# Performance work log

Measured on AMD Instinct MI355X. Metric: run time of the kernel, lower is better.

## Reference

```python
import jax, jax.numpy as jnp
import numpy as np

B, FEAT, SPD_H, CTRL_H, N_CMD = 32768, 512, 128, 256, 4


def _p(key, shape, fan_in):
    # torch nn.Linear default init: U(-1/sqrt(fan_in), 1/sqrt(fan_in))
    lim = 1.0 / np.sqrt(fan_in)
    return jax.random.uniform(key, shape, jnp.float32, -lim, lim)


def setup_inputs() -> dict:
    key = jax.random.key(0)
    ks = iter(jax.random.split(key, 32))
    inp = {
        "feat": jax.random.normal(next(ks), (B, FEAT), jnp.float32),
        "speed": jax.random.uniform(next(ks), (B,), jnp.float32),
        "command": jax.random.randint(next(ks), (B,), 0, N_CMD, jnp.int32),
        "ms_w1": _p(next(ks), (1, SPD_H), 1), "ms_b1": _p(next(ks), (SPD_H,), 1),
        "ms_w2": _p(next(ks), (SPD_H, SPD_H), SPD_H), "ms_b2": _p(next(ks), (SPD_H,), SPD_H),
        "ms_w3": _p(next(ks), (SPD_H, SPD_H), SPD_H), "ms_b3": _p(next(ks), (SPD_H,), SPD_H),
        # speed_pred_module: 512 -> 256 -> 256 -> 1
        "sp_w1": _p(next(ks), (FEAT, CTRL_H), FEAT), "sp_b1": _p(next(ks), (CTRL_H,), FEAT),
        "sp_w2": _p(next(ks), (CTRL_H, CTRL_H), CTRL_H), "sp_b2": _p(next(ks), (CTRL_H,), CTRL_H),
        "sp_w3": _p(next(ks), (CTRL_H, 1), CTRL_H), "sp_b3": _p(next(ks), (1,), CTRL_H),
        # join_module: Linear(640, 512)
        "join_w": _p(next(ks), (FEAT + SPD_H, FEAT), FEAT + SPD_H),
        "join_b": _p(next(ks), (FEAT,), FEAT + SPD_H),
        # 4 control heads: 512 -> 256 -> 256 -> 3 (stacked on expert axis e)
        "ctrl_w1": _p(next(ks), (N_CMD, FEAT, CTRL_H), FEAT), "ctrl_b1": _p(next(ks), (N_CMD, CTRL_H), FEAT),
        "ctrl_w2": _p(next(ks), (N_CMD, CTRL_H, CTRL_H), CTRL_H), "ctrl_b2": _p(next(ks), (N_CMD, CTRL_H), CTRL_H),
        "ctrl_w3": _p(next(ks), (N_CMD, CTRL_H, 3), CTRL_H), "ctrl_b3": _p(next(ks), (N_CMD, 3), CTRL_H),
    }
    return inp


def _mlp(x, w1, b1, w2, b2, w3, b3):
    # FullyConnectedNet: Linear, ReLU, Linear, Dropout(p=0 -> noop), ReLU, Linear
    h = jax.nn.relu(x @ w1 + b1)
    h = jax.nn.relu(h @ w2 + b2)
    return h @ w3 + b3


def reference(feat, speed, command,
              ms_w1, ms_b1, ms_w2, ms_b2, ms_w3, ms_b3,
              sp_w1, sp_b1, sp_w2, sp_b2, sp_w3, sp_b3,
              join_w, join_b,
              ctrl_w1, ctrl_b1, ctrl_w2, ctrl_b2, ctrl_w3, ctrl_b3):
    v = _mlp(speed[:, None], ms_w1, ms_b1, ms_w2, ms_b2, ms_w3, ms_b3)      # [B,128]
    joined = jnp.concatenate([feat, v], axis=1) @ join_w + join_b           # [B,512]
    v_p = _mlp(feat, sp_w1, sp_b1, sp_w2, sp_b2, sp_w3, sp_b3)              # [B,1]
    # command-indexed dispatch: compute all 4 heads densely, then select per sample
    h1 = jax.nn.relu(jnp.einsum('bd,edh->beh', joined, ctrl_w1) + ctrl_b1)  # [B,4,256]
    h2 = jax.nn.relu(jnp.einsum('beh,ehk->bek', h1, ctrl_w2) + ctrl_b2)     # [B,4,256]
    act_all = jnp.einsum('bek,eko->beo', h2, ctrl_w3) + ctrl_b3             # [B,4,3]
    action = jnp.take_along_axis(act_all, command[:, None, None].astype(jnp.int32), axis=1)[:, 0]  # [B,3]
    throttle = jax.nn.sigmoid(action[:, 0])
    steering = jnp.tanh(action[:, 1])
    brake = jax.nn.sigmoid(action[:, 2])
    return v_p, throttle, brake, steering
```

## Files before the change

kernel.cpp:

```cpp
#include <hip/hip_runtime.h>
#include <hip/hip_bf16.h>
#include <stdint.h>
#include <math.h>

#define BB 32768
#define FEAT 512
#define SPD_H 128
#define CTRL_H 256
#define NCMD 4

typedef __attribute__((ext_vector_type(8))) short bf16x8;
typedef __attribute__((ext_vector_type(4))) float f32x4;

__device__ __forceinline__ unsigned short f2bf(float f) {
  union { float f; uint32_t u; } v; v.f = f;
  uint32_t u = v.u;
  return (unsigned short)((u + 0x7fffu + ((u >> 16) & 1u)) >> 16);
}

__device__ __forceinline__ void async16(const unsigned short* g, unsigned short* l) {
  __builtin_amdgcn_global_load_lds(
      (const __attribute__((address_space(1))) unsigned int*)g,
      (__attribute__((address_space(3))) unsigned int*)l, 16, 0, 0);
}

__device__ __forceinline__ void gemm128(
    const unsigned short* __restrict__ A, int lda,
    const int* __restrict__ perm, int m_start, int m_cnt,
    const unsigned short* __restrict__ W, const float* __restrict__ bi,
    unsigned short* __restrict__ C, int ldc, int relu, int K, int mt, int nt) {
  extern __shared__ __align__(16) unsigned char dynsm[];
  unsigned short* As = (unsigned short*)dynsm;
  unsigned short* Bs = As + 128 * 32;

  const int m0 = mt * 128;
  if (m0 >= m_cnt) return;
  const int n0 = nt * 128;
  const int t = threadIdx.x;
  const int w = t >> 6, lane = t & 63;
  const int wm = w & 1, wn = w >> 1;

  f32x4 acc[4][4];
#pragma unroll
  for (int i = 0; i < 4; ++i)
#pragma unroll
    for (int j = 0; j < 4; ++j)
#pragma unroll
      for (int r = 0; r < 4; ++r) acc[i][j][r] = 0.f;

  const int fr = lane & 15;
  const int fk = (lane >> 4) * 8;

  const unsigned short* agp[2]; const unsigned short* bgp[2];
  unsigned short* al[2]; unsigned short* bl[2];
#pragma unroll
  for (int it = 0; it < 2; ++it) {
    int row = w * 32 + it * 16 + (lane >> 2);
    int seg8 = (lane & 3) * 8;
    int rl = m0 + row;
    if (rl >= m_cnt) rl = m_cnt - 1;
    int grow = perm ? perm[m_start + rl] : (m_start + rl);
    agp[it] = A + (size_t)grow * lda + seg8;
    bgp[it] = W + (size_t)(n0 + row) * K + seg8;
    al[it] = As + (w * 32 + it * 16) * 32;
    bl[it] = Bs + (w * 32 + it * 16) * 32;
  }

  for (int k0 = 0; k0 < K; k0 += 32) {
#pragma unroll
    for (int it = 0; it < 2; ++it) {
      async16(agp[it] + k0, al[it]);
      async16(bgp[it] + k0, bl[it]);
    }
    __syncthreads();
    bf16x8 af[4], bfv[4];
#pragma unroll
    for (int i = 0; i < 4; ++i)
      af[i] = *(const bf16x8*)(As + (wm * 64 + i * 16 + fr) * 32 + fk);
#pragma unroll
    for (int j = 0; j < 4; ++j)
      bfv[j] = *(const bf16x8*)(Bs + (wn * 64 + j * 16 + fr) * 32 + fk);
#pragma unroll
    for (int i = 0; i < 4; ++i)
#pragma unroll
      for (int j = 0; j < 4; ++j)
        acc[i][j] = __builtin_amdgcn_mfma_f32_16x16x32_bf16(af[i], bfv[j], acc[i][j], 0, 0, 0);
    __syncthreads();
  }

  const int rquad = (lane >> 4) * 4;
  const int cidx = lane & 15;

  float bv[4];
#pragma unroll
  for (int j = 0; j < 4; ++j) bv[j] = bi ? bi[n0 + wn * 64 + j * 16 + cidx] : 0.f;

  unsigned short (*bscr)[136] = (unsigned short(*)[136])dynsm;
#pragma unroll
  for (int c = 0; c < 4; ++c) {
    if (wm == (c >> 1)) {
#pragma unroll
      for (int j = 0; j < 4; ++j) {
#pragma unroll
        for (int ii = 0; ii < 2; ++ii) {
          int i = 2 * (c & 1) + ii;
          int lr = ii * 16 + rquad;
#pragma unroll
          for (int r = 0; r < 4; ++r) {
            float v = acc[i][j][r] + bv[j];
            if (relu) v = fmaxf(v, 0.f);
            bscr[lr + r][wn * 64 + j * 16 + cidx] = f2bf(v);
          }
        }
      }
    }
    __syncthreads();
#pragma unroll
    for (int q = 0; q < 2; ++q) {
      int sg = t + 256 * q;
      int lr = sg >> 4, cs = (sg & 15) * 8;
      int grow = m0 + c * 32 + lr;
      if (grow < m_cnt)
        *(bf16x8*)(C + (size_t)(m_start + grow) * ldc + (n0 + cs)) =
            *(const bf16x8*)(&bscr[lr][cs]);
    }
    __syncthreads();
  }
}

struct WSeg { const float* src; unsigned short* dst; int K; int N; int ldd; };
struct PrepArgs {
  WSeg s[12];
  int start[13];
  const float* join_w; unsigned short* wjbf;
  const float* feat; unsigned short* ajoin;
  const int* cmd; int* wavecnt;
  const float* join_b; const float* ctrl_w1; const float* ctrl_b1; float* b_f;
};
__launch_bounds__(256)
__global__ void k_prep(PrepArgs a) {
  int bx = blockIdx.x, t = threadIdx.x;
  if (bx < 16384) {
    int idx = bx * 256 + t;
    int i = idx >> 7;
    int j4 = (idx & 127) << 2;
    float4 f = *(const float4*)(a.feat + (size_t)i * FEAT + j4);
    ushort4 o;
    o.x = f2bf(f.x); o.y = f2bf(f.y); o.z = f2bf(f.z); o.w = f2bf(f.w);
    *(ushort4*)(a.ajoin + (size_t)i * 640 + j4) = o;
    return;
  }
  int rel = bx - 16384;
  if (rel < 320) {
    int idx = rel * 256 + t;
    float4 f = *(const float4*)(a.join_w + (size_t)idx * 4);
    ushort4 o;
    o.x = f2bf(f.x); o.y = f2bf(f.y); o.z = f2bf(f.z); o.w = f2bf(f.w);
    *(ushort4*)(a.wjbf + (size_t)idx * 4) = o;
    return;
  }
  rel -= 320;
  if (rel < a.start[12]) {
    __shared__ float tb[32][33];
    int si = 0;
    while (rel >= a.start[si + 1]) ++si;
    WSeg sg = a.s[si];
    int tile = rel - a.start[si];
    int tkx = sg.K >> 5;
    int tn = tile / tkx;
    int tk = tile - tn * tkx;
    int k0 = tk * 32, n0 = tn * 32;
    int tx = t & 31, ty = t >> 5;
#pragma unroll
    for (int j = 0; j < 4; ++j)
      tb[ty + j * 8][tx] = sg.src[(size_t)(k0 + ty + j * 8) * sg.N + n0 + tx];
    __syncthreads();
#pragma unroll
    for (int j = 0; j < 4; ++j)
      sg.dst[(size_t)(n0 + ty + j * 8) * sg.ldd + k0 + tx] = f2bf(tb[tx][ty + j * 8]);
    return;
  }
  rel -= a.start[12];
  if (rel < 128) {
    int i = rel * 256 + t;
    int c = a.cmd[i];
    int wid = i >> 6;
    int lane = t & 63;
#pragma unroll
    for (int cv = 0; cv < NCMD; ++cv) {
      unsigned long long m = __ballot(c == cv);
      if (lane == 0) a.wavecnt[cv * 512 + wid] = __popcll(m);
    }
    return;
  }
  int e = rel - 128;
  float s = a.ctrl_b1[e * 256 + t];
  const float* w = a.ctrl_w1 + (size_t)e * 512 * 256 + t;
  for (int m = 0; m < 512; ++m) s = fmaf(a.join_b[m], w[(size_t)m * 256], s);
  a.b_f[e * 256 + t] = s;
}

struct MidArgs {
  const int* cmd; const int* wavecnt; int* perm; int* offs;
  const unsigned short* c_w1t; const unsigned short* wjbf; unsigned short* wf_t;
  const float* speed;
  const float* ms_w1; const float* ms_b1;
  const unsigned short* ms_w2t; const float* ms_b2;
  const unsigned short* ms_w3t; const float* ms_b3;
  unsigned short* ajoin;
};
__launch_bounds__(256)
__global__ void k_mid(MidArgs a) {
  int b = blockIdx.x, t = threadIdx.x;
  if (b >= 168) {
    extern __shared__ __align__(16) unsigned char dynsm[];
    unsigned short (*hw)[136] = (unsigned short(*)[136])dynsm;
    unsigned short* BsM = (unsigned short*)(dynsm + 128 * 136 * 2);
    const int m0 = (b - 168) * 128;
    const int w = t >> 6, lane = t & 63;
    const int wm = w & 1, wn = w >> 1;
    const int fr = lane & 15, fk = (lane >> 4) * 8;
    const int rquad = (lane >> 4) * 4, cidx = lane & 15;
    {
      int r = t >> 1, half = t & 1;
      float s = a.speed[m0 + r];
#pragma unroll
      for (int c0 = 0; c0 < 64; c0 += 4) {
        int c = half * 64 + c0;
        float4 wv = *(const float4*)(a.ms_w1 + c);
        float4 bv = *(const float4*)(a.ms_b1 + c);
        hw[r][c + 0] = f2bf(fmaxf(fmaf(s, wv.x, bv.x), 0.f));
        hw[r][c + 1] = f2bf(fmaxf(fmaf(s, wv.y, bv.y), 0.f));
        hw[r][c + 2] = f2bf(fmaxf(fmaf(s, wv.z, bv.z), 0.f));
        hw[r][c + 3] = f2bf(fmaxf(fmaf(s, wv.w, bv.w), 0.f));
      }
    }
    __syncthreads();
    for (int layer = 0; layer < 2; ++layer) {
      const unsigned short* Wt = layer ? a.ms_w3t : a.ms_w2t;
      const float* bb = layer ? a.ms_b3 : a.ms_b2;
      f32x4 acc[4][4];
#pragma unroll
      for (int i = 0; i < 4; ++i)
#pragma unroll
        for (int j = 0; j < 4; ++j)
#pragma unroll
          for (int r = 0; r < 4; ++r) acc[i][j][r] = 0.f;
      for (int k0 = 0; k0 < 128; k0 += 32) {
#pragma unroll
        for (int it = 0; it < 2; ++it) {
          int row = w * 32 + it * 16 + (lane >> 2);
          async16(Wt + (size_t)row * 128 + k0 + (lane & 3) * 8,
                  BsM + (w * 32 + it * 16) * 32);
        }
        __syncthreads();
        bf16x8 af[4], bfv[4];
#pragma unroll
        for (int i = 0; i < 4; ++i)
          af[i] = *(const bf16x8*)(&hw[wm * 64 + i * 16 + fr][k0 + fk]);
#pragma unroll
        for (int j = 0; j < 4; ++j)
          bfv[j] = *(const bf16x8*)(BsM + (wn * 64 + j * 16 + fr) * 32 + fk);
#pragma unroll
        for (int i = 0; i < 4; ++i)
#pragma unroll
          for (int j = 0; j < 4; ++j)
            acc[i][j] = __builtin_amdgcn_mfma_f32_16x16x32_bf16(af[i], bfv[j], acc[i][j], 0, 0, 0);
        __syncthreads();
      }
#pragma unroll
      for (int j = 0; j < 4; ++j) {
        int col = wn * 64 + j * 16 + cidx;
        float bv = bb[col];
#pragma unroll
        for (int i = 0; i < 4; ++i) {
          int row = wm * 64 + i * 16 + rquad;
#pragma unroll
          for (int r = 0; r < 4; ++r) {
            float v = acc[i][j][r] + bv;
            if (layer == 0) v = fmaxf(v, 0.f);
            hw[row + r][col] = f2bf(v);
          }
        }
      }
      __syncthreads();
    }
    {
      int r = t >> 1, half = t & 1;
#pragma unroll
      for (int c8 = 0; c8 < 8; ++c8)
        *(bf16x8*)(a.ajoin + (size_t)(m0 + r) * 640 + 512 + half * 64 + c8 * 8) =
            *(const bf16x8*)(&hw[r][half * 64 + c8 * 8]);
    }
    return;
  }
  if (b >= 128) {
    int idx = b - 128;
    int mt = idx & 7, nt = idx >> 3;
    gemm128(a.c_w1t, 512, nullptr, 0, 1024, a.wjbf, nullptr, a.wf_t, 640, 0, 512, mt, nt);
    return;
  }
  __shared__ int pf[NCMD][4];
  __shared__ int tot[NCMD];
  int c = t >> 6, lane = t & 63;
  int v[8]; int s = 0;
#pragma unroll
  for (int q = 0; q < 8; ++q) { v[q] = a.wavecnt[c * 512 + lane * 8 + q]; s += v[q]; }
  int p = s;
#pragma unroll
  for (int m = 1; m < 64; m <<= 1) { int o = __shfl_up(p, m, 64); if (lane >= m) p += o; }
  int excl = p - s;
  if (lane == 63) tot[c] = p;
  if (lane == ((4 * b) >> 3)) {
    int base_off = (4 * b) & 7;
    int run = excl;
#pragma unroll
    for (int q = 0; q < 8; ++q) {
      if (q >= base_off && q < base_off + 4) pf[c][q - base_off] = run;
      run += v[q];
    }
  }
  __syncthreads();
  int soffs[NCMD + 1];
  soffs[0] = 0;
#pragma unroll
  for (int e = 0; e < NCMD; ++e) soffs[e + 1] = soffs[e] + tot[e];
  if (b == 0 && t == 0)
    for (int e = 0; e <= NCMD; ++e) a.offs[e] = soffs[e];
  int i = b * 256 + t;
  int mc = a.cmd[i];
  int lwid = t >> 6;
  int rank = 0, base = 0;
#pragma unroll
  for (int cv = 0; cv < NCMD; ++cv) {
    unsigned long long m = __ballot(mc == cv);
    if (mc == cv) {
      rank = __popcll(m & ((1ull << lane) - 1ull));
      base = soffs[cv] + pf[cv][lwid];
    }
  }
  a.perm[base + rank] = i;
}

struct MainArgs {
  const unsigned short* ajoin;
  const unsigned short* wf_t; const float* b_f;
  const unsigned short* sp_w1t; const float* sp_b1;
  unsigned short* ch1; unsigned short* sph1p;
  const int* perm; const int* seg;
};
__launch_bounds__(256)
__global__ void k_main(MainArgs a) {
  const int e = blockIdx.z;
  const int gid = blockIdx.x;
  const int mt = gid & 255, nt = gid >> 8;
  int ms = a.seg[e], mc = a.seg[e + 1] - ms;
  if (nt < 2) {
    gemm128(a.ajoin, 640, a.perm, ms, mc, a.wf_t + (size_t)e * 256 * 640,
            a.b_f + e * 256, a.ch1, 256, 1, 640, mt, nt);
  } else {
    gemm128(a.ajoin, 640, a.perm, ms, mc, a.sp_w1t, a.sp_b1,
            a.sph1p, 256, 1, 512, mt, nt - 2);
  }
}

struct VArgs {
  const unsigned short* A_s; const unsigned short* A_c;
  const unsigned short* W_s; const unsigned short* W_c;
  const float* b_s; const float* b_c;
  const float* w3_s; const float* b3_s;
  const float* w3_c; const float* b3_c;
  const int* perm; const int* seg;
  float* out;
};
__launch_bounds__(256)
__global__ void k_vgemm(VArgs a) {
  __shared__ unsigned short As[64 * 32];
  __shared__ unsigned short Bs[256 * 32];
  const int z = blockIdx.z;
  const unsigned short* A; const unsigned short* W; const float* bi;
  int m_start, m_cnt;
  if (z == 4) { A = a.A_s; W = a.W_s; bi = a.b_s; m_start = 0; m_cnt = BB; }
  else {
    A = a.A_c; W = a.W_c + (size_t)z * 65536; bi = a.b_c + z * 256;
    m_start = a.seg[z]; m_cnt = a.seg[z + 1] - m_start;
  }
  const int m0 = blockIdx.x * 64;
  if (m0 >= m_cnt) return;
  const int t = threadIdx.x, w = t >> 6, lane = t & 63;
  const int fr = lane & 15, fk = (lane >> 4) * 8;

  f32x4 acc[16];
#pragma unroll
  for (int j = 0; j < 16; ++j)
#pragma unroll
    for (int r = 0; r < 4; ++r) acc[j][r] = 0.f;

  int arow = m0 + w * 16 + (lane >> 2);
  if (arow >= m_cnt) arow = m_cnt - 1;
  const unsigned short* ap = A + (size_t)(m_start + arow) * 256 + (lane & 3) * 8;
  unsigned short* al = As + (w * 16) * 32;
  const unsigned short* bp[4]; unsigned short* bl[4];
#pragma unroll
  for (int it = 0; it < 4; ++it) {
    int brow = w * 64 + it * 16 + (lane >> 2);
    bp[it] = W + (size_t)brow * 256 + (lane & 3) * 8;
    bl[it] = Bs + (w * 64 + it * 16) * 32;
  }

  for (int k0 = 0; k0 < 256; k0 += 32) {
    async16(ap + k0, al);
#pragma unroll
    for (int it = 0; it < 4; ++it) async16(bp[it] + k0, bl[it]);
    __syncthreads();
    bf16x8 af = *(const bf16x8*)(As + (w * 16 + fr) * 32 + fk);
#pragma unroll
    for (int j = 0; j < 16; ++j) {
      bf16x8 bfv = *(const bf16x8*)(Bs + (j * 16 + fr) * 32 + fk);
      acc[j] = __builtin_amdgcn_mfma_f32_16x16x32_bf16(af, bfv, acc[j], 0, 0, 0);
    }
    __syncthreads();
  }

  const int rquad = (lane >> 4) * 4;
  float bcol[16];
#pragma unroll
  for (int j = 0; j < 16; ++j) bcol[j] = bi[j * 16 + fr];

  if (z == 4) {
    float aw[16];
#pragma unroll
    for (int j = 0; j < 16; ++j) aw[j] = a.w3_s[j * 16 + fr];
#pragma unroll
    for (int r = 0; r < 4; ++r) {
      float s = 0.f;
#pragma unroll
      for (int j = 0; j < 16; ++j)
        s = fmaf(fmaxf(acc[j][r] + bcol[j], 0.f), aw[j], s);
      s += __shfl_xor(s, 1, 64);
      s += __shfl_xor(s, 2, 64);
      s += __shfl_xor(s, 4, 64);
      s += __shfl_xor(s, 8, 64);
      int row = m0 + w * 16 + rquad + r;
      if (fr == 0 && row < m_cnt)
        a.out[a.perm[row]] = s + a.b3_s[0];
    }
  } else {
    float aw0[16], aw1[16], aw2[16];
#pragma unroll
    for (int j = 0; j < 16; ++j) {
      const float* wp = a.w3_c + (size_t)z * 768 + (j * 16 + fr) * 3;
      aw0[j] = wp[0]; aw1[j] = wp[1]; aw2[j] = wp[2];
    }
#pragma unroll
    for (int r = 0; r < 4; ++r) {
      float s0 = 0.f, s1 = 0.f, s2 = 0.f;
#pragma unroll
      for (int j = 0; j < 16; ++j) {
        float v = fmaxf(acc[j][r] + bcol[j], 0.f);
        s0 = fmaf(v, aw0[j], s0);
        s1 = fmaf(v, aw1[j], s1);
        s2 = fmaf(v, aw2[j], s2);
      }
#pragma unroll
      for (int m = 1; m <= 8; m <<= 1) {
        s0 += __shfl_xor(s0, m, 64);
        s1 += __shfl_xor(s1, m, 64);
        s2 += __shfl_xor(s2, m, 64);
      }
      int row = m0 + w * 16 + rquad + r;
      if (fr == 0 && row < m_cnt) {
        int orig = a.perm[m_start + row];
        float a0 = s0 + a.b3_c[z * 3 + 0];
        float a1 = s1 + a.b3_c[z * 3 + 1];
        float a2 = s2 + a.b3_c[z * 3 + 2];
        a.out[BB + orig]     = 1.f / (1.f + __expf(-a0));
        a.out[2 * BB + orig] = 1.f / (1.f + __expf(-a2));
        a.out[3 * BB + orig] = tanhf(a1);
      }
    }
  }
}

static inline size_t align256(size_t x) { return (x + 255) & ~(size_t)255; }

extern "C" void kernel_launch(void* const* d_in, const int* in_sizes, int n_in,
                              void* d_out, int out_size, void* d_ws, size_t ws_size,
                              hipStream_t stream) {
  const float* feat   = (const float*)d_in[0];
  const float* speed  = (const float*)d_in[1];
  const int*   command= (const int*)d_in[2];
  const float* ms_w1  = (const float*)d_in[3];
  const float* ms_b1  = (const float*)d_in[4];
  const float* ms_w2  = (const float*)d_in[5];
  const float* ms_b2  = (const float*)d_in[6];
  const float* ms_w3  = (const float*)d_in[7];
  const float* ms_b3  = (const float*)d_in[8];
  const float* sp_w1  = (const float*)d_in[9];
  const float* sp_b1  = (const float*)d_in[10];
  const float* sp_w2  = (const float*)d_in[11];
  const float* sp_b2  = (const float*)d_in[12];
  const float* sp_w3  = (const float*)d_in[13];
  const float* sp_b3  = (const float*)d_in[14];
  const float* join_w = (const float*)d_in[15];
  const float* join_b = (const float*)d_in[16];
  const float* ctrl_w1= (const float*)d_in[17];
  const float* ctrl_b1= (const float*)d_in[18];
  const float* ctrl_w2= (const float*)d_in[19];
  const float* ctrl_b2= (const float*)d_in[20];
  const float* ctrl_w3= (const float*)d_in[21];
  const float* ctrl_b3= (const float*)d_in[22];
  float* out = (float*)d_out;

  char* ws = (char*)d_ws;
  size_t off = 0;
  auto alloc = [&](size_t bytes) -> char* { char* p = ws + off; off = align256(off + bytes); return p; };

  unsigned short* ajoin  = (unsigned short*)alloc((size_t)BB * 640 * 2);
  unsigned short* sph1p  = (unsigned short*)alloc((size_t)BB * 256 * 2);
  unsigned short* ch1    = (unsigned short*)alloc((size_t)BB * 256 * 2);
  unsigned short* wtp    = (unsigned short*)alloc(1998848ull * 2);
  int* perm    = (int*)alloc((size_t)BB * 4);
  int* cnt     = (int*)alloc(64);
  int* wavecnt = (int*)alloc(4 * 512 * 4);
  float* b_f   = (float*)alloc(4 * 256 * 4);

  unsigned short* sp_w1t = wtp;
  unsigned short* sp_w2t = wtp + 131072;
  unsigned short* ms_w2t = wtp + 196608;
  unsigned short* ms_w3t = wtp + 212992;
  unsigned short* c_w1t  = wtp + 229376;
  unsigned short* c_w2t  = wtp + 753664;
  unsigned short* wjbf   = wtp + 1015808;
  unsigned short* wf_t   = wtp + 1343488;

  PrepArgs P;
  P.s[0] = { sp_w1, sp_w1t, 512, 256, 512 };
  P.s[1] = { sp_w2, sp_w2t, 256, 256, 256 };
  P.s[2] = { ms_w2, ms_w2t, 128, 128, 128 };
  P.s[3] = { ms_w3, ms_w3t, 128, 128, 128 };
  for (int e = 0; e < 4; ++e) P.s[4 + e] = { ctrl_w1 + (size_t)e * 512 * 256, c_w1t + (size_t)e * 131072, 512, 256, 512 };
  for (int e = 0; e < 4; ++e) P.s[8 + e] = { ctrl_w2 + (size_t)e * 256 * 256, c_w2t + (size_t)e * 65536, 256, 256, 256 };
  P.start[0] = 0;
  for (int i = 0; i < 12; ++i)
    P.start[i + 1] = P.start[i] + (P.s[i].K >> 5) * (P.s[i].N >> 5);
  P.join_w = join_w; P.wjbf = wjbf;
  P.feat = feat; P.ajoin = ajoin;
  P.cmd = command; P.wavecnt = wavecnt;
  P.join_b = join_b; P.ctrl_w1 = ctrl_w1; P.ctrl_b1 = ctrl_b1; P.b_f = b_f;
  int prep_blocks = 16384 + 320 + P.start[12] + 128 + 4;

  k_prep<<<prep_blocks, 256, 0, stream>>>(P);

  MidArgs Mi;
  Mi.cmd = command; Mi.wavecnt = wavecnt; Mi.perm = perm; Mi.offs = cnt + 4;
  Mi.c_w1t = c_w1t; Mi.wjbf = wjbf; Mi.wf_t = wf_t;
  Mi.speed = speed;
  Mi.ms_w1 = ms_w1; Mi.ms_b1 = ms_b1;
  Mi.ms_w2t = ms_w2t; Mi.ms_b2 = ms_b2;
  Mi.ms_w3t = ms_w3t; Mi.ms_b3 = ms_b3;
  Mi.ajoin = ajoin;
  k_mid<<<168 + 256, 256, 128 * 136 * 2 + 128 * 32 * 2, stream>>>(Mi);

  MainArgs Ma;
  Ma.ajoin = ajoin; Ma.wf_t = wf_t; Ma.b_f = b_f;
  Ma.sp_w1t = sp_w1t; Ma.sp_b1 = sp_b1;
  Ma.ch1 = ch1; Ma.sph1p = sph1p;
  Ma.perm = perm; Ma.seg = cnt + 4;
  k_main<<<dim3(1024, 1, 4), 256, 128 * 32 * 2 * 2, stream>>>(Ma);

  VArgs V;
  V.A_s = sph1p; V.A_c = ch1; V.W_s = sp_w2t; V.W_c = c_w2t;
  V.b_s = sp_b2; V.b_c = ctrl_b2;
  V.w3_s = sp_w3; V.b3_s = sp_b3; V.w3_c = ctrl_w3; V.b3_c = ctrl_b3;
  V.perm = perm; V.seg = cnt + 4; V.out = out;
  k_vgemm<<<dim3(512, 1, 5), 256, 0, stream>>>(V);
}
```

Before: 232.8 us.

## Fuse layer-1 and layer-2 GEMMs into one tail kernel with compact expert tiles

Replaces the separate first-layer GEMM kernel and second-layer GEMM kernel with a single k_tail kernel. Each block computes a 64-row tile's hidden layer into swizzled LDS, then runs the second GEMM and the final projection directly from it. This removes the global round trip of the two B×256 intermediate activations and one launch. Expert tiles are now enumerated compactly from the per-command counts rather than launched over a padded grid with early exits. The trade-offs are that B weights are read straight from global memory without LDS staging, and the bias-fold loop is split into four accumulators.

```diff
diff --git a/kernel.cpp b/kernel.cpp
--- a/kernel.cpp
+++ b/kernel.cpp
@@ -194,10 +194,16 @@
     return;
   }
   int e = rel - 128;
-  float s = a.ctrl_b1[e * 256 + t];
+  float s0 = a.ctrl_b1[e * 256 + t], s1 = 0.f, s2 = 0.f, s3 = 0.f;
   const float* w = a.ctrl_w1 + (size_t)e * 512 * 256 + t;
-  for (int m = 0; m < 512; ++m) s = fmaf(a.join_b[m], w[(size_t)m * 256], s);
-  a.b_f[e * 256 + t] = s;
+#pragma unroll 4
+  for (int m = 0; m < 512; m += 4) {
+    s0 = fmaf(a.join_b[m + 0], w[(size_t)(m + 0) * 256], s0);
+    s1 = fmaf(a.join_b[m + 1], w[(size_t)(m + 1) * 256], s1);
+    s2 = fmaf(a.join_b[m + 2], w[(size_t)(m + 2) * 256], s2);
+    s3 = fmaf(a.join_b[m + 3], w[(size_t)(m + 3) * 256], s3);
+  }
+  a.b_f[e * 256 + t] = (s0 + s1) + (s2 + s3);
 }
 
 struct MidArgs {
@@ -208,6 +214,7 @@
   const unsigned short* ms_w2t; const float* ms_b2;
   const unsigned short* ms_w3t; const float* ms_b3;
   unsigned short* ajoin;
+  int* tile_e; int* tile_r0; int* ntl;
 };
 __launch_bounds__(256)
 __global__ void k_mid(MidArgs a) {
@@ -340,143 +347,230 @@
     }
   }
   a.perm[base + rank] = i;
+
+  if (b == 0) {
+    int toff[NCMD + 1];
+    toff[0] = 0;
+#pragma unroll
+    for (int ee = 0; ee < NCMD; ++ee) toff[ee + 1] = toff[ee] + ((tot[ee] + 63) >> 6);
+    if (t == 0) a.ntl[0] = toff[NCMD];
+    for (int ti = t; ti < toff[NCMD]; ti += 256) {
+      int ee = 0;
+      while (ti >= toff[ee + 1]) ++ee;
+      a.tile_e[ti] = ee;
+      a.tile_r0[ti] = soffs[ee] + (ti - toff[ee]) * 64;
+    }
+  }
 }
 
-struct MainArgs {
+struct TailArgs {
   const unsigned short* ajoin;
-  const unsigned short* wf_t; const float* b_f;
+  const unsigned short* wf_t;  const float* b_f;
   const unsigned short* sp_w1t; const float* sp_b1;
-  unsigned short* ch1; unsigned short* sph1p;
+  const unsigned short* c_w2t; const float* ctrl_b2;
+  const unsigned short* sp_w2t; const float* sp_b2;
+  const float* ctrl_w3; const float* ctrl_b3;
+  const float* sp_w3; const float* sp_b3;
   const int* perm; const int* seg;
-};
-__launch_bounds__(256)
-__global__ void k_main(MainArgs a) {
-  const int e = blockIdx.z;
-  const int gid = blockIdx.x;
-  const int mt = gid & 255, nt = gid >> 8;
-  int ms = a.seg[e], mc = a.seg[e + 1] - ms;
-  if (nt < 2) {
-    gemm128(a.ajoin, 640, a.perm, ms, mc, a.wf_t + (size_t)e * 256 * 640,
-            a.b_f + e * 256, a.ch1, 256, 1, 640, mt, nt);
-  } else {
-    gemm128(a.ajoin, 640, a.perm, ms, mc, a.sp_w1t, a.sp_b1,
-            a.sph1p, 256, 1, 512, mt, nt - 2);
-  }
-}
-
-struct VArgs {
-  const unsigned short* A_s; const unsigned short* A_c;
-  const unsigned short* W_s; const unsigned short* W_c;
-  const float* b_s; const float* b_c;
-  const float* w3_s; const float* b3_s;
-  const float* w3_c; const float* b3_c;
-  const int* perm; const int* seg;
+  const int* tile_e; const int* tile_r0; const int* ntl;
   float* out;
 };
-__launch_bounds__(256)
-__global__ void k_vgemm(VArgs a) {
-  __shared__ unsigned short As[64 * 32];
-  __shared__ unsigned short Bs[256 * 32];
-  const int z = blockIdx.z;
-  const unsigned short* A; const unsigned short* W; const float* bi;
-  int m_start, m_cnt;
-  if (z == 4) { A = a.A_s; W = a.W_s; bi = a.b_s; m_start = 0; m_cnt = BB; }
-  else {
-    A = a.A_c; W = a.W_c + (size_t)z * 65536; bi = a.b_c + z * 256;
-    m_start = a.seg[z]; m_cnt = a.seg[z + 1] - m_start;
-  }
-  const int m0 = blockIdx.x * 64;
-  if (m0 >= m_cnt) return;
-  const int t = threadIdx.x, w = t >> 6, lane = t & 63;
-  const int fr = lane & 15, fk = (lane >> 4) * 8;
-
-  f32x4 acc[16];
-#pragma unroll
-  for (int j = 0; j < 16; ++j)
-#pragma unroll
-    for (int r = 0; r < 4; ++r) acc[j][r] = 0.f;
-
-  int arow = m0 + w * 16 + (lane >> 2);
-  if (arow >= m_cnt) arow = m_cnt - 1;
-  const unsigned short* ap = A + (size_t)(m_start + arow) * 256 + (lane & 3) * 8;
-  unsigned short* al = As + (w * 16) * 32;
-  const unsigned short* bp[4]; unsigned short* bl[4];
-#pragma unroll
-  for (int it = 0; it < 4; ++it) {
-    int brow = w * 64 + it * 16 + (lane >> 2);
-    bp[it] = W + (size_t)brow * 256 + (lane & 3) * 8;
-    bl[it] = Bs + (w * 64 + it * 16) * 32;
-  }
-
+__launch_bounds__(256, 3)
+__global__ void k_tail(TailArgs a) {
+  extern __shared__ __align__(16) unsigned char dynsm[];
+  unsigned short* As = (unsigned short*)dynsm;
+  unsigned short* h1 = (unsigned short*)(dynsm + 16384);
+  float* pscr = (float*)dynsm;
+
+  const int t = threadIdx.x;
+  const int w = t >> 6, lane = t & 63;
+  const int fr = lane & 15, fcg = lane >> 4;
+  const int rquad = fcg * 4, cidx = fr;
+  const int fkS = ((fcg ^ (fr & 3)) << 3);
+
+  int is_sp, e = 0, NC;
+  const unsigned short *W1, *W2;
+  const float *b1, *b2;
+  int r0, rend;
+  if (blockIdx.x < 512) {
+    is_sp = 1; NC = 8;
+    W1 = a.sp_w1t; W2 = a.sp_w2t; b1 = a.sp_b1; b2 = a.sp_b2;
+    r0 = blockIdx.x * 64; rend = BB;
+  } else {
+    int ti = blockIdx.x - 512;
+    if (ti >= a.ntl[0]) return;
+    is_sp = 0; e = a.tile_e[ti]; NC = 10;
+    W1 = a.wf_t + (size_t)e * 256 * 640;
+    W2 = a.c_w2t + (size_t)e * 65536;
+    b1 = a.b_f + e * 256; b2 = a.ctrl_b2 + e * 256;
+    r0 = a.tile_r0[ti]; rend = a.seg[e + 1];
+  }
+  const int K = is_sp ? 512 : 640;
+
+  const unsigned short* agp[2];
+  {
+    int rl = r0 + w * 16 + (lane >> 2);
+    if (rl >= rend) rl = rend - 1;
+    int grow = is_sp ? rl : a.perm[rl];
+    const unsigned short* g0 =
+        a.ajoin + (size_t)grow * 640 + (((lane & 3) ^ ((lane >> 2) & 3)) << 3);
+    agp[0] = g0; agp[1] = g0 + 32;
+  }
+  unsigned short* alb0 = As + w * 16 * 32;
+  unsigned short* alb1 = As + 2048 + w * 16 * 32;
+
+  const unsigned short* bp[4];
+#pragma unroll
+  for (int j = 0; j < 4; ++j)
+    bp[j] = W1 + (size_t)(w * 64 + j * 16 + fr) * K + fcg * 8;
+
+  f32x4 acc[4][4];
+#pragma unroll
+  for (int i = 0; i < 4; ++i)
+#pragma unroll
+    for (int j = 0; j < 4; ++j)
+#pragma unroll
+      for (int r = 0; r < 4; ++r) acc[i][j][r] = 0.f;
+
+  async16(agp[0], alb0);
+  async16(agp[1], alb1);
+
+  for (int c = 0; c < NC; ++c) {
+    const int cur = (c & 1) * 4096;
+    if (c + 1 < NC) {
+      const int nb = ((c + 1) & 1) * 4096;
+      async16(agp[0] + (c + 1) * 64, alb0 + nb);
+      async16(agp[1] + (c + 1) * 64, alb1 + nb);
+      asm volatile("s_waitcnt vmcnt(2)" ::: "memory");
+    } else {
+      asm volatile("s_waitcnt vmcnt(0)" ::: "memory");
+    }
+    __builtin_amdgcn_s_barrier();
+#pragma unroll
+    for (int ks = 0; ks < 2; ++ks) {
+      const int k0 = c * 64 + ks * 32;
+      bf16x8 af[4], bv[4];
+#pragma unroll
+      for (int i = 0; i < 4; ++i)
+        af[i] = *(const bf16x8*)(As + cur + ks * 2048 + (i * 16 + fr) * 32 + fkS);
+#pragma unroll
+      for (int j = 0; j < 4; ++j)
+        bv[j] = *(const bf16x8*)(bp[j] + k0);
+#pragma unroll
+      for (int i = 0; i < 4; ++i)
+#pragma unroll
+        for (int j = 0; j < 4; ++j)
+          acc[i][j] = __builtin_amdgcn_mfma_f32_16x16x32_bf16(af[i], bv[j], acc[i][j], 0, 0, 0);
+    }
+    __builtin_amdgcn_s_barrier();
+  }
+
+#pragma unroll
+  for (int j = 0; j < 4; ++j) {
+    const int col = w * 64 + j * 16 + cidx;
+    const float bj = b1[col];
+    const int c8 = col >> 3, cl = col & 7;
+#pragma unroll
+    for (int i = 0; i < 4; ++i) {
+#pragma unroll
+      for (int r = 0; r < 4; ++r) {
+        const int row = i * 16 + rquad + r;
+        h1[(row << 8) + (((c8 ^ (row & 7)) << 3) | cl)] =
+            f2bf(fmaxf(acc[i][j][r] + bj, 0.f));
+      }
+    }
+  }
+  __syncthreads();
+
+  const unsigned short* bp2[4];
+#pragma unroll
+  for (int j = 0; j < 4; ++j)
+    bp2[j] = W2 + (size_t)(w * 64 + j * 16 + fr) * 256 + fcg * 8;
+
+#pragma unroll
+  for (int i = 0; i < 4; ++i)
+#pragma unroll
+    for (int j = 0; j < 4; ++j)
+#pragma unroll
+      for (int r = 0; r < 4; ++r) acc[i][j][r] = 0.f;
+
+#pragma unroll 2
   for (int k0 = 0; k0 < 256; k0 += 32) {
-    async16(ap + k0, al);
-#pragma unroll
-    for (int it = 0; it < 4; ++it) async16(bp[it] + k0, bl[it]);
-    __syncthreads();
-    bf16x8 af = *(const bf16x8*)(As + (w * 16 + fr) * 32 + fk);
-#pragma unroll
-    for (int j = 0; j < 16; ++j) {
-      bf16x8 bfv = *(const bf16x8*)(Bs + (j * 16 + fr) * 32 + fk);
-      acc[j] = __builtin_amdgcn_mfma_f32_16x16x32_bf16(af, bfv, acc[j], 0, 0, 0);
-    }
-    __syncthreads();
-  }
-
-  const int rquad = (lane >> 4) * 4;
-  float bcol[16];
-#pragma unroll
-  for (int j = 0; j < 16; ++j) bcol[j] = bi[j * 16 + fr];
-
-  if (z == 4) {
-    float aw[16];
-#pragma unroll
-    for (int j = 0; j < 16; ++j) aw[j] = a.w3_s[j * 16 + fr];
-#pragma unroll
-    for (int r = 0; r < 4; ++r) {
-      float s = 0.f;
-#pragma unroll
-      for (int j = 0; j < 16; ++j)
-        s = fmaf(fmaxf(acc[j][r] + bcol[j], 0.f), aw[j], s);
-      s += __shfl_xor(s, 1, 64);
-      s += __shfl_xor(s, 2, 64);
-      s += __shfl_xor(s, 4, 64);
-      s += __shfl_xor(s, 8, 64);
-      int row = m0 + w * 16 + rquad + r;
-      if (fr == 0 && row < m_cnt)
-        a.out[a.perm[row]] = s + a.b3_s[0];
-    }
-  } else {
-    float aw0[16], aw1[16], aw2[16];
-#pragma unroll
-    for (int j = 0; j < 16; ++j) {
-      const float* wp = a.w3_c + (size_t)z * 768 + (j * 16 + fr) * 3;
-      aw0[j] = wp[0]; aw1[j] = wp[1]; aw2[j] = wp[2];
-    }
+    bf16x8 af[4], bv[4];
+#pragma unroll
+    for (int i = 0; i < 4; ++i) {
+      const int row = i * 16 + fr;
+      const int c8 = (k0 >> 3) + fcg;
+      af[i] = *(const bf16x8*)(h1 + (row << 8) + ((c8 ^ (row & 7)) << 3));
+    }
+#pragma unroll
+    for (int j = 0; j < 4; ++j)
+      bv[j] = *(const bf16x8*)(bp2[j] + k0);
+#pragma unroll
+    for (int i = 0; i < 4; ++i)
+#pragma unroll
+      for (int j = 0; j < 4; ++j)
+        acc[i][j] = __builtin_amdgcn_mfma_f32_16x16x32_bf16(af[i], bv[j], acc[i][j], 0, 0, 0);
+  }
+
+  float b2v[4], w30[4], w31[4], w32[4];
+#pragma unroll
+  for (int j = 0; j < 4; ++j) {
+    const int col = w * 64 + j * 16 + cidx;
+    b2v[j] = b2[col];
+    if (is_sp) {
+      w30[j] = a.sp_w3[col]; w31[j] = 0.f; w32[j] = 0.f;
+    } else {
+      const float* wp = a.ctrl_w3 + (size_t)e * 768 + col * 3;
+      w30[j] = wp[0]; w31[j] = wp[1]; w32[j] = wp[2];
+    }
+  }
+#pragma unroll
+  for (int i = 0; i < 4; ++i) {
 #pragma unroll
     for (int r = 0; r < 4; ++r) {
       float s0 = 0.f, s1 = 0.f, s2 = 0.f;
 #pragma unroll
-      for (int j = 0; j < 16; ++j) {
-        float v = fmaxf(acc[j][r] + bcol[j], 0.f);
-        s0 = fmaf(v, aw0[j], s0);
-        s1 = fmaf(v, aw1[j], s1);
-        s2 = fmaf(v, aw2[j], s2);
+      for (int j = 0; j < 4; ++j) {
+        const float v = fmaxf(acc[i][j][r] + b2v[j], 0.f);
+        s0 = fmaf(v, w30[j], s0);
+        if (!is_sp) { s1 = fmaf(v, w31[j], s1); s2 = fmaf(v, w32[j], s2); }
       }
 #pragma unroll
       for (int m = 1; m <= 8; m <<= 1) {
         s0 += __shfl_xor(s0, m, 64);
-        s1 += __shfl_xor(s1, m, 64);
-        s2 += __shfl_xor(s2, m, 64);
-      }
-      int row = m0 + w * 16 + rquad + r;
-      if (fr == 0 && row < m_cnt) {
-        int orig = a.perm[m_start + row];
-        float a0 = s0 + a.b3_c[z * 3 + 0];
-        float a1 = s1 + a.b3_c[z * 3 + 1];
-        float a2 = s2 + a.b3_c[z * 3 + 2];
-        a.out[BB + orig]     = 1.f / (1.f + __expf(-a0));
-        a.out[2 * BB + orig] = 1.f / (1.f + __expf(-a2));
-        a.out[3 * BB + orig] = tanhf(a1);
+        if (!is_sp) { s1 += __shfl_xor(s1, m, 64); s2 += __shfl_xor(s2, m, 64); }
+      }
+      if (cidx == 0) {
+        const int row = i * 16 + rquad + r;
+        pscr[(row * 4 + w) * 3 + 0] = s0;
+        if (!is_sp) {
+          pscr[(row * 4 + w) * 3 + 1] = s1;
+          pscr[(row * 4 + w) * 3 + 2] = s2;
+        }
+      }
+    }
+  }
+  __syncthreads();
+
+  if (is_sp) {
+    if (t < 64) {
+      float s = pscr[t * 12] + pscr[t * 12 + 3] + pscr[t * 12 + 6] + pscr[t * 12 + 9]
+              + a.sp_b3[0];
+      a.out[r0 + t] = s;
+    }
+  } else {
+    if (t < 192) {
+      const int row = t / 3, o = t - row * 3;
+      const int rl = r0 + row;
+      if (rl < rend) {
+        float s = pscr[row * 12 + o] + pscr[row * 12 + 3 + o] +
+                  pscr[row * 12 + 6 + o] + pscr[row * 12 + 9 + o] +
+                  a.ctrl_b3[e * 3 + o];
+        const int orig = a.perm[rl];
+        if (o == 0)      a.out[BB + orig]     = 1.f / (1.f + __expf(-s));
+        else if (o == 2) a.out[2 * BB + orig] = 1.f / (1.f + __expf(-s));
+        else             a.out[3 * BB + orig] = tanhf(s);
       }
     }
   }
@@ -517,13 +611,14 @@
   auto alloc = [&](size_t bytes) -> char* { char* p = ws + off; off = align256(off + bytes); return p; };
 
   unsigned short* ajoin  = (unsigned short*)alloc((size_t)BB * 640 * 2);
-  unsigned short* sph1p  = (unsigned short*)alloc((size_t)BB * 256 * 2);
-  unsigned short* ch1    = (unsigned short*)alloc((size_t)BB * 256 * 2);
   unsigned short* wtp    = (unsigned short*)alloc(1998848ull * 2);
   int* perm    = (int*)alloc((size_t)BB * 4);
   int* cnt     = (int*)alloc(64);
   int* wavecnt = (int*)alloc(4 * 512 * 4);
   float* b_f   = (float*)alloc(4 * 256 * 4);
+  int* tile_e  = (int*)alloc(520 * 4);
+  int* tile_r0 = (int*)alloc(520 * 4);
+  int* ntl     = (int*)alloc(64);
 
   unsigned short* sp_w1t = wtp;
   unsigned short* sp_w2t = wtp + 131072;
@@ -560,19 +655,18 @@
   Mi.ms_w2t = ms_w2t; Mi.ms_b2 = ms_b2;
   Mi.ms_w3t = ms_w3t; Mi.ms_b3 = ms_b3;
   Mi.ajoin = ajoin;
+  Mi.tile_e = tile_e; Mi.tile_r0 = tile_r0; Mi.ntl = ntl;
   k_mid<<<168 + 256, 256, 128 * 136 * 2 + 128 * 32 * 2, stream>>>(Mi);
 
-  MainArgs Ma;
-  Ma.ajoin = ajoin; Ma.wf_t = wf_t; Ma.b_f = b_f;
-  Ma.sp_w1t = sp_w1t; Ma.sp_b1 = sp_b1;
-  Ma.ch1 = ch1; Ma.sph1p = sph1p;
-  Ma.perm = perm; Ma.seg = cnt + 4;
-  k_main<<<dim3(1024, 1, 4), 256, 128 * 32 * 2 * 2, stream>>>(Ma);
-
-  VArgs V;
-  V.A_s = sph1p; V.A_c = ch1; V.W_s = sp_w2t; V.W_c = c_w2t;
-  V.b_s = sp_b2; V.b_c = ctrl_b2;
-  V.w3_s = sp_w3; V.b3_s = sp_b3; V.w3_c = ctrl_w3; V.b3_c = ctrl_b3;
-  V.perm = perm; V.seg = cnt + 4; V.out = out;
-  k_vgemm<<<dim3(512, 1, 5), 256, 0, stream>>>(V);
+  TailArgs T;
+  T.ajoin = ajoin; T.wf_t = wf_t; T.b_f = b_f;
+  T.sp_w1t = sp_w1t; T.sp_b1 = sp_b1;
+  T.c_w2t = c_w2t; T.ctrl_b2 = ctrl_b2;
+  T.sp_w2t = sp_w2t; T.sp_b2 = sp_b2;
+  T.ctrl_w3 = ctrl_w3; T.ctrl_b3 = ctrl_b3;
+  T.sp_w3 = sp_w3; T.sp_b3 = sp_b3;
+  T.perm = perm; T.seg = cnt + 4;
+  T.tile_e = tile_e; T.tile_r0 = tile_r0; T.ntl = ntl;
+  T.out = out;
+  k_tail<<<dim3(512 + 516), 256, 49152, stream>>>(T);
 }
```

New measurement: 240.7 us. 3.4% more time.
